# Kernel optimization log

Measured on AMD Instinct MI355X. Metric: run time of the kernel, lower is better.

Reference implementation:

```python
import jax, jax.numpy as jnp
import numpy as np

DIM = 2048
BATCH = 64


def setup_inputs() -> dict:
    key = jax.random.key(0)
    kx, kq, kk, kv = jax.random.split(key, 4)
    s = 1.0 / np.sqrt(DIM).astype(np.float32)  # keep q*k logits O(1)
    x = jax.random.normal(kx, (BATCH, DIM), dtype=jnp.float32)
    Wq = jax.random.normal(kq, (DIM, DIM), dtype=jnp.float32) * s
    Wk = jax.random.normal(kk, (DIM, DIM), dtype=jnp.float32) * s
    Wv = jax.random.normal(kv, (DIM, DIM), dtype=jnp.float32) * s
    return {"x": x, "Wq": Wq, "Wk": Wk, "Wv": Wv}


def reference(x, Wq, Wk, Wv):
    # nn.Linear(dim, inner_dim, bias=False): y = x @ W.T, W: [inner_dim, dim]
    q = x @ Wq.T  # [b, N]  (head_dim = 1, so each token's q is a scalar)
    k = x @ Wk.T  # [b, N]
    v = x @ Wv.T  # [b, N]
    # dot[b,i,j] = q[b,i] * k[b,j]  (rank-1 outer product per batch)
    logits = q[:, :, None] * k[:, None, :]  # [b, N, N]
    attn = jax.nn.softmax(logits, axis=-1)
    out = jnp.einsum("bij,bj->bi", attn, v)  # [b, N]
    # dim == inner_dim -> scale is Identity
    return out
```

## Files before the change

kernel.cpp:

```cpp
#include <hip/hip_runtime.h>
#include <hip/hip_bf16.h>

#define DIM 2048
#define NB  64
#define KSL 8
#define KT  256
#define JSL 4

typedef short bf16x8 __attribute__((ext_vector_type(8)));
typedef short s16x4  __attribute__((ext_vector_type(4)));
typedef float f32x4  __attribute__((ext_vector_type(4)));
typedef float f32x2  __attribute__((ext_vector_type(2)));

__device__ __forceinline__ unsigned short f32_to_bf16_rne(float f) {
  unsigned u = __builtin_bit_cast(unsigned, f);
  unsigned r = u + 0x7FFF + ((u >> 16) & 1);
  return (unsigned short)(r >> 16);
}

__global__ __launch_bounds__(256)
void prep(const float* __restrict__ x, unsigned short* __restrict__ xrh,
          unsigned short* __restrict__ xrl) {
  const int tg = blockIdx.x * 256 + threadIdx.x;
  const int b = tg >> 9;
  const int k = (tg & 511) * 4;
  float4 f = *(const float4*)(x + (size_t)b * DIM + k);
  const int mt = b >> 4, l15 = b & 15;
  const int ck = k >> 5, quad = (k >> 3) & 3, u = k & 7;
  const size_t off = (((size_t)(mt * 64 + ck) * 64) + quad * 16 + l15) * 8 + u;
  float vf[4] = {f.x, f.y, f.z, f.w};
  ushort4 h4, l4;
  unsigned short* hp = &h4.x;
  unsigned short* lp = &l4.x;
#pragma unroll
  for (int e = 0; e < 4; ++e) {
    unsigned short h = f32_to_bf16_rne(vf[e]);
    float hf = __builtin_bit_cast(float, ((unsigned)h) << 16);
    hp[e] = h;
    lp[e] = f32_to_bf16_rne(vf[e] - hf);
  }
  *(ushort4*)(xrh + off) = h4;
  *(ushort4*)(xrl + off) = l4;
}

__global__ __launch_bounds__(256)
void qkv_mfma(const unsigned short* __restrict__ xrh,
              const unsigned short* __restrict__ xrl,
              const float* __restrict__ Wq, const float* __restrict__ Wk,
              const float* __restrict__ Wv, float* __restrict__ part) {
  const int mat = blockIdx.z;
  const float* __restrict__ W = (mat == 0) ? Wq : ((mat == 1) ? Wk : Wv);
  const int t = threadIdx.x;
  const int wave = t >> 6, lane = t & 63;
  const int l15 = lane & 15, quad = lane >> 4;
  const int j0 = blockIdx.x * 32;
  const int kb0 = blockIdx.y * KT;

  __shared__ short wh[32][264];
  __shared__ short wl[32][264];

#pragma unroll
  for (int p = 0; p < 8; ++p) {
    const int r = p * 4 + wave;
    float4 w4 = *(const float4*)(W + (size_t)(j0 + r) * DIM + kb0 + lane * 4);
    float wf[4] = {w4.x, w4.y, w4.z, w4.w};
    s16x4 h4, l4;
#pragma unroll
    for (int e = 0; e < 4; ++e) {
      unsigned uu = __builtin_bit_cast(unsigned, wf[e]);
      h4[e] = (short)(uu >> 16);
      float hf = __builtin_bit_cast(float, uu & 0xFFFF0000u);
      float res = wf[e] - hf;
      l4[e] = (short)(__builtin_bit_cast(unsigned, res) >> 16);
    }
    *(s16x4*)&wh[r][lane * 4] = h4;
    *(s16x4*)&wl[r][lane * 4] = l4;
  }
  __syncthreads();

  const int jh = wave & 1;
  const int mh = wave >> 1;
  f32x4 acc[2] = {{0.f,0.f,0.f,0.f},{0.f,0.f,0.f,0.f}};

#pragma unroll
  for (int kk = 0; kk < 8; ++kk) {
    bf16x8 whf = *(const bf16x8*)&wh[jh * 16 + l15][kk * 32 + quad * 8];
    bf16x8 wlf = *(const bf16x8*)&wl[jh * 16 + l15][kk * 32 + quad * 8];
    const int ck = blockIdx.y * 8 + kk;
#pragma unroll
    for (int u = 0; u < 2; ++u) {
      const int mt = mh * 2 + u;
      const size_t xo = (((size_t)(mt * 64 + ck)) * 64 + lane) * 8;
      bf16x8 ah = *(const bf16x8*)(xrh + xo);
      bf16x8 al = *(const bf16x8*)(xrl + xo);
      acc[u] = __builtin_amdgcn_mfma_f32_16x16x32_bf16(ah, whf, acc[u], 0, 0, 0);
      acc[u] = __builtin_amdgcn_mfma_f32_16x16x32_bf16(al, whf, acc[u], 0, 0, 0);
      acc[u] = __builtin_amdgcn_mfma_f32_16x16x32_bf16(ah, wlf, acc[u], 0, 0, 0);
    }
  }

  float* __restrict__ pb =
      part + ((size_t)(blockIdx.y * 3 + mat) * NB) * DIM + j0 + jh * 16 + l15;
#pragma unroll
  for (int u = 0; u < 2; ++u)
#pragma unroll
    for (int r = 0; r < 4; ++r) {
      const int b = (mh * 2 + u) * 16 + quad * 4 + r;
      pb[(size_t)b * DIM] = acc[u][r];
    }
}

__global__ __launch_bounds__(256)
void reduce_qkv(const float* __restrict__ part, float* __restrict__ qkv) {
  const size_t i2 = ((size_t)blockIdx.x * 256 + threadIdx.x) * 2;
  float2 s = make_float2(0.f, 0.f);
#pragma unroll
  for (int sl = 0; sl < KSL; ++sl) {
    float2 p = *(const float2*)(part + (size_t)sl * 3 * NB * DIM + i2);
    s.x += p.x; s.y += p.y;
  }
  *(float2*)(qkv + i2) = s;
}

__global__ __launch_bounds__(256)
void attn(const float* __restrict__ qkv, f32x2* __restrict__ pnd) {
  const int b = blockIdx.z, js = blockIdx.y, t = threadIdx.x;
  const int i = blockIdx.x * 256 + t;
  const int jb = js * (DIM / JSL), j2 = t * 2;

  __shared__ __align__(16) float ks[DIM / JSL];
  __shared__ __align__(16) float vs[DIM / JSL];

  *(float2*)(ks + j2) = *(const float2*)(qkv + ((size_t)(NB + b)) * DIM + jb + j2);
  *(float2*)(vs + j2) = *(const float2*)(qkv + ((size_t)(2 * NB + b)) * DIM + jb + j2);
  const float qi = qkv[(size_t)b * DIM + i];
  __syncthreads();

  const float c = qi * 1.4426950408889634f;
  f32x2 num0 = {0.f, 0.f}, num1 = {0.f, 0.f};
  f32x2 den0 = {0.f, 0.f}, den1 = {0.f, 0.f};
#pragma unroll 4
  for (int j = 0; j < DIM / JSL; j += 8) {
    float4 k0 = *(const float4*)(ks + j);
    float4 k1 = *(const float4*)(ks + j + 4);
    float4 v0 = *(const float4*)(vs + j);
    float4 v1 = *(const float4*)(vs + j + 4);
    f32x2 e0, e1, e2, e3;
    e0.x = __builtin_amdgcn_exp2f(c * k0.x);
    e0.y = __builtin_amdgcn_exp2f(c * k0.y);
    e1.x = __builtin_amdgcn_exp2f(c * k0.z);
    e1.y = __builtin_amdgcn_exp2f(c * k0.w);
    e2.x = __builtin_amdgcn_exp2f(c * k1.x);
    e2.y = __builtin_amdgcn_exp2f(c * k1.y);
    e3.x = __builtin_amdgcn_exp2f(c * k1.z);
    e3.y = __builtin_amdgcn_exp2f(c * k1.w);
    den0 += e0; den1 += e1; den0 += e2; den1 += e3;
    f32x2 va = {v0.x, v0.y}, vb = {v0.z, v0.w};
    f32x2 vc = {v1.x, v1.y}, vd = {v1.z, v1.w};
    num0 = __builtin_elementwise_fma(e0, va, num0);
    num1 = __builtin_elementwise_fma(e1, vb, num1);
    num0 = __builtin_elementwise_fma(e2, vc, num0);
    num1 = __builtin_elementwise_fma(e3, vd, num1);
  }
  f32x2 nd;
  nd.x = (num0.x + num0.y) + (num1.x + num1.y);
  nd.y = (den0.x + den0.y) + (den1.x + den1.y);
  pnd[((size_t)b * JSL + js) * DIM + i] = nd;
}

__global__ __launch_bounds__(256)
void attn_fin(const f32x2* __restrict__ pnd, float* __restrict__ out) {
  const int b = blockIdx.y;
  const int i = blockIdx.x * 256 + threadIdx.x;
  float n = 0.f, d = 0.f;
#pragma unroll
  for (int s = 0; s < JSL; ++s) {
    f32x2 p = pnd[((size_t)b * JSL + s) * DIM + i];
    n += p.x; d += p.y;
  }
  out[(size_t)b * DIM + i] = n / d;
}

extern "C" void kernel_launch(void* const* d_in, const int* in_sizes, int n_in,
                              void* d_out, int out_size, void* d_ws, size_t ws_size,
                              hipStream_t stream) {
  const float* x  = (const float*)d_in[0];
  const float* Wq = (const float*)d_in[1];
  const float* Wk = (const float*)d_in[2];
  const float* Wv = (const float*)d_in[3];
  float* out = (float*)d_out;

  char* w = (char*)d_ws;
  unsigned short* xrh = (unsigned short*)w;
  unsigned short* xrl = (unsigned short*)(w + (512 << 10));
  float* part = (float*)(w + (1 << 20));
  float* qkv  = (float*)(w + (16 << 20));
  f32x2* pnd  = (f32x2*)(w + (20 << 20));

  hipLaunchKernelGGL(prep, dim3(128), dim3(256), 0, stream, x, xrh, xrl);
  hipLaunchKernelGGL(qkv_mfma, dim3(64, KSL, 3), dim3(256), 0, stream,
                     xrh, xrl, Wq, Wk, Wv, part);
  hipLaunchKernelGGL(reduce_qkv, dim3(768), dim3(256), 0, stream, part, qkv);
  hipLaunchKernelGGL(attn, dim3(8, JSL, NB), dim3(256), 0, stream, qkv, pnd);
  hipLaunchKernelGGL(attn_fin, dim3(8, NB), dim3(256), 0, stream, pnd, out);
}
```

Before: 140.6 us.

## Fuse split-K reduction into attention load and double-buffer weight loads

Halves the number of split-K slices in the QKV projection, so each block covers 512 of the K dimension in two 256-wide chunks. The second chunk's weights are prefetched into registers while the first chunk is converted and multiplied. The separate reduce_qkv kernel is removed, and the attention kernel sums the partial q/k/v slices directly as it loads them. This saves one kernel launch and one round trip through global memory, at the cost of fewer blocks in the GEMM, more register pressure from the prefetch, and redundant partial-sum reads across attention blocks. The LDS row stride also changes and the fragment loads are split into 64-bit halves.

```diff
diff --git a/kernel.cpp b/kernel.cpp
--- a/kernel.cpp
+++ b/kernel.cpp
@@ -3,8 +3,7 @@
 
 #define DIM 2048
 #define NB  64
-#define KSL 8
-#define KT  256
+#define KSL 4
 #define JSL 4
 
 typedef short bf16x8 __attribute__((ext_vector_type(8)));
@@ -43,6 +42,28 @@
   *(ushort4*)(xrl + off) = l4;
 }
 
+#define WSTR 260
+
+__device__ __forceinline__ void conv_store_w(short (*wh)[WSTR], short (*wl)[WSTR],
+                                             const float4* wreg, int wave, int lane) {
+#pragma unroll
+  for (int p = 0; p < 8; ++p) {
+    const int r = p * 4 + wave;
+    float wf[4] = {wreg[p].x, wreg[p].y, wreg[p].z, wreg[p].w};
+    s16x4 h4, l4;
+#pragma unroll
+    for (int e = 0; e < 4; ++e) {
+      unsigned uu = __builtin_bit_cast(unsigned, wf[e]);
+      h4[e] = (short)(uu >> 16);
+      float hf = __builtin_bit_cast(float, uu & 0xFFFF0000u);
+      float res = wf[e] - hf;
+      l4[e] = (short)(__builtin_bit_cast(unsigned, res) >> 16);
+    }
+    *(s16x4*)&wh[r][lane * 4] = h4;
+    *(s16x4*)&wl[r][lane * 4] = l4;
+  }
+}
+
 __global__ __launch_bounds__(256)
 void qkv_mfma(const unsigned short* __restrict__ xrh,
               const unsigned short* __restrict__ xrl,
@@ -54,49 +75,54 @@
   const int wave = t >> 6, lane = t & 63;
   const int l15 = lane & 15, quad = lane >> 4;
   const int j0 = blockIdx.x * 32;
-  const int kb0 = blockIdx.y * KT;
-
-  __shared__ short wh[32][264];
-  __shared__ short wl[32][264];
-
-#pragma unroll
-  for (int p = 0; p < 8; ++p) {
-    const int r = p * 4 + wave;
-    float4 w4 = *(const float4*)(W + (size_t)(j0 + r) * DIM + kb0 + lane * 4);
-    float wf[4] = {w4.x, w4.y, w4.z, w4.w};
-    s16x4 h4, l4;
-#pragma unroll
-    for (int e = 0; e < 4; ++e) {
-      unsigned uu = __builtin_bit_cast(unsigned, wf[e]);
-      h4[e] = (short)(uu >> 16);
-      float hf = __builtin_bit_cast(float, uu & 0xFFFF0000u);
-      float res = wf[e] - hf;
-      l4[e] = (short)(__builtin_bit_cast(unsigned, res) >> 16);
-    }
-    *(s16x4*)&wh[r][lane * 4] = h4;
-    *(s16x4*)&wl[r][lane * 4] = l4;
-  }
-  __syncthreads();
+  const int kb0 = blockIdx.y * 512;
+
+  __shared__ __align__(16) short wh[32][WSTR];
+  __shared__ __align__(16) short wl[32][WSTR];
 
   const int jh = wave & 1;
   const int mh = wave >> 1;
+  const int frow = jh * 16 + l15;
   f32x4 acc[2] = {{0.f,0.f,0.f,0.f},{0.f,0.f,0.f,0.f}};
 
-#pragma unroll
-  for (int kk = 0; kk < 8; ++kk) {
-    bf16x8 whf = *(const bf16x8*)&wh[jh * 16 + l15][kk * 32 + quad * 8];
-    bf16x8 wlf = *(const bf16x8*)&wl[jh * 16 + l15][kk * 32 + quad * 8];
-    const int ck = blockIdx.y * 8 + kk;
-#pragma unroll
-    for (int u = 0; u < 2; ++u) {
-      const int mt = mh * 2 + u;
-      const size_t xo = (((size_t)(mt * 64 + ck)) * 64 + lane) * 8;
-      bf16x8 ah = *(const bf16x8*)(xrh + xo);
-      bf16x8 al = *(const bf16x8*)(xrl + xo);
-      acc[u] = __builtin_amdgcn_mfma_f32_16x16x32_bf16(ah, whf, acc[u], 0, 0, 0);
-      acc[u] = __builtin_amdgcn_mfma_f32_16x16x32_bf16(al, whf, acc[u], 0, 0, 0);
-      acc[u] = __builtin_amdgcn_mfma_f32_16x16x32_bf16(ah, wlf, acc[u], 0, 0, 0);
-    }
+  float4 wa[8], wb[8];
+#pragma unroll
+  for (int p = 0; p < 8; ++p)
+    wa[p] = *(const float4*)(W + (size_t)(j0 + p * 4 + wave) * DIM + kb0 + lane * 4);
+
+#pragma unroll
+  for (int c = 0; c < 2; ++c) {
+    if (c == 0) conv_store_w(wh, wl, wa, wave, lane);
+    else        conv_store_w(wh, wl, wb, wave, lane);
+    if (c == 0) {
+#pragma unroll
+      for (int p = 0; p < 8; ++p)
+        wb[p] = *(const float4*)(W + (size_t)(j0 + p * 4 + wave) * DIM +
+                                 kb0 + 256 + lane * 4);
+    }
+    __syncthreads();
+
+    const int ckb = blockIdx.y * 16 + c * 8;
+#pragma unroll
+    for (int kk = 0; kk < 8; ++kk) {
+      bf16x8 whf, wlf;
+      *(s16x4*)&whf       = *(const s16x4*)&wh[frow][kk * 32 + quad * 8];
+      *(((s16x4*)&whf)+1) = *(const s16x4*)&wh[frow][kk * 32 + quad * 8 + 4];
+      *(s16x4*)&wlf       = *(const s16x4*)&wl[frow][kk * 32 + quad * 8];
+      *(((s16x4*)&wlf)+1) = *(const s16x4*)&wl[frow][kk * 32 + quad * 8 + 4];
+      const int ck = ckb + kk;
+#pragma unroll
+      for (int u = 0; u < 2; ++u) {
+        const int mt = mh * 2 + u;
+        const size_t xo = (((size_t)(mt * 64 + ck)) * 64 + lane) * 8;
+        bf16x8 ah = *(const bf16x8*)(xrh + xo);
+        bf16x8 al = *(const bf16x8*)(xrl + xo);
+        acc[u] = __builtin_amdgcn_mfma_f32_16x16x32_bf16(ah, whf, acc[u], 0, 0, 0);
+        acc[u] = __builtin_amdgcn_mfma_f32_16x16x32_bf16(al, whf, acc[u], 0, 0, 0);
+        acc[u] = __builtin_amdgcn_mfma_f32_16x16x32_bf16(ah, wlf, acc[u], 0, 0, 0);
+      }
+    }
+    if (c == 0) __syncthreads();
   }
 
   float* __restrict__ pb =
@@ -111,19 +137,7 @@
 }
 
 __global__ __launch_bounds__(256)
-void reduce_qkv(const float* __restrict__ part, float* __restrict__ qkv) {
-  const size_t i2 = ((size_t)blockIdx.x * 256 + threadIdx.x) * 2;
-  float2 s = make_float2(0.f, 0.f);
-#pragma unroll
-  for (int sl = 0; sl < KSL; ++sl) {
-    float2 p = *(const float2*)(part + (size_t)sl * 3 * NB * DIM + i2);
-    s.x += p.x; s.y += p.y;
-  }
-  *(float2*)(qkv + i2) = s;
-}
-
-__global__ __launch_bounds__(256)
-void attn(const float* __restrict__ qkv, f32x2* __restrict__ pnd) {
+void attn(const float* __restrict__ part, f32x2* __restrict__ pnd) {
   const int b = blockIdx.z, js = blockIdx.y, t = threadIdx.x;
   const int i = blockIdx.x * 256 + t;
   const int jb = js * (DIM / JSL), j2 = t * 2;
@@ -131,9 +145,18 @@
   __shared__ __align__(16) float ks[DIM / JSL];
   __shared__ __align__(16) float vs[DIM / JSL];
 
-  *(float2*)(ks + j2) = *(const float2*)(qkv + ((size_t)(NB + b)) * DIM + jb + j2);
-  *(float2*)(vs + j2) = *(const float2*)(qkv + ((size_t)(2 * NB + b)) * DIM + jb + j2);
-  const float qi = qkv[(size_t)b * DIM + i];
+  float kx = 0.f, ky = 0.f, vx = 0.f, vy = 0.f, qi = 0.f;
+#pragma unroll
+  for (int sl = 0; sl < KSL; ++sl) {
+    const float* __restrict__ pk = part + ((size_t)(sl * 3 + 1) * NB + b) * DIM + jb;
+    const float* __restrict__ pv = part + ((size_t)(sl * 3 + 2) * NB + b) * DIM + jb;
+    float2 a  = *(const float2*)(pk + j2);
+    float2 c2 = *(const float2*)(pv + j2);
+    kx += a.x; ky += a.y; vx += c2.x; vy += c2.y;
+    qi += part[((size_t)(sl * 3 + 0) * NB + b) * DIM + i];
+  }
+  *(float2*)(ks + j2) = make_float2(kx, ky);
+  *(float2*)(vs + j2) = make_float2(vx, vy);
   __syncthreads();
 
   const float c = qi * 1.4426950408889634f;
@@ -194,13 +217,11 @@
   unsigned short* xrh = (unsigned short*)w;
   unsigned short* xrl = (unsigned short*)(w + (512 << 10));
   float* part = (float*)(w + (1 << 20));
-  float* qkv  = (float*)(w + (16 << 20));
-  f32x2* pnd  = (f32x2*)(w + (20 << 20));
+  f32x2* pnd  = (f32x2*)(w + (16 << 20));
 
   hipLaunchKernelGGL(prep, dim3(128), dim3(256), 0, stream, x, xrh, xrl);
   hipLaunchKernelGGL(qkv_mfma, dim3(64, KSL, 3), dim3(256), 0, stream,
                      xrh, xrl, Wq, Wk, Wv, part);
-  hipLaunchKernelGGL(reduce_qkv, dim3(768), dim3(256), 0, stream, part, qkv);
-  hipLaunchKernelGGL(attn, dim3(8, JSL, NB), dim3(256), 0, stream, qkv, pnd);
+  hipLaunchKernelGGL(attn, dim3(8, JSL, NB), dim3(256), 0, stream, part, pnd);
   hipLaunchKernelGGL(attn_fin, dim3(8, NB), dim3(256), 0, stream, pnd, out);
 }
```

Result: faster. 133.8 us (-4.9%).
